# Kernel tuning notes

Measured on AMD Instinct MI355X. Metric: run time of the kernel, lower is better.

## Reference

```python
import jax, jax.numpy as jnp
import numpy as np

BS, CS, PS, D_INPUT, H, D = 4, 1024, 1024, 1024, 16, 64
T = CS + PS  # total key length
SCALE = 1.0 / D ** 0.5


def _rel_shift(x):
    # x: (bs, cs, T, H) -- faithful reshape-based relative shift
    zero_pad = jnp.zeros((*x.shape[:2], 1, x.shape[-1]), dtype=x.dtype)
    return jnp.concatenate([zero_pad, x], axis=2).reshape(
        (x.shape[2] + 1, *x.shape[:2], x.shape[-1]))[1:].reshape(x.shape)


def setup_inputs() -> dict:
    key = jax.random.key(0)
    ks = jax.random.split(key, 9)
    s = 1.0 / np.sqrt(D_INPUT)
    input_ = jax.random.normal(ks[0], (BS, CS, D_INPUT), jnp.float32)
    pos_embs = jax.random.normal(ks[1], (T, D_INPUT), jnp.float32)
    memory = jax.random.normal(ks[2], (BS, PS, D_INPUT), jnp.float32)
    u = jax.random.normal(ks[3], (H, D), jnp.float32) * 0.02
    v = jax.random.normal(ks[4], (H, D), jnp.float32) * 0.02
    W_kv = jax.random.normal(ks[5], (D_INPUT, 2 * H * D), jnp.float32) * s
    W_q = jax.random.normal(ks[6], (D_INPUT, H * D), jnp.float32) * s
    W_p = jax.random.normal(ks[7], (D_INPUT, H * D), jnp.float32) * s
    W_out = jax.random.normal(ks[8], (H * D, D_INPUT), jnp.float32) * (1.0 / np.sqrt(H * D))
    # causal mask: query i may attend to key j iff j <= i + prev_seq. True = keep.
    mask = (jnp.arange(T)[None, :] <= jnp.arange(CS)[:, None] + PS)[..., None]  # (cs, T, 1)
    return {"input_": input_, "pos_embs": pos_embs, "memory": memory,
            "u": u, "v": v, "W_kv": W_kv, "W_q": W_q, "W_p": W_p,
            "W_out": W_out, "mask": mask}


def reference(input_, pos_embs, memory, u, v, W_kv, W_q, W_p, W_out, mask):
    bs, cs, _ = input_.shape
    ps = memory.shape[1]
    t = cs + ps
    input_with_memory = jnp.concatenate([memory, input_], axis=1)  # (bs, T, d_input)
    kv = input_with_memory @ W_kv                                  # (bs, T, 2*H*D)
    k_tfmd, v_tfmd = jnp.split(kv, 2, axis=-1)
    q_tfmd = input_ @ W_q                                          # (bs, cs, H*D)
    q = q_tfmd.reshape(bs, cs, H, D)
    k = k_tfmd.reshape(bs, t, H, D)
    content_attn = jnp.einsum('bihd,bjhd->bijh', q + u, k)
    p_tfmd = (pos_embs @ W_p).reshape(t, H, D)
    position_attn = jnp.einsum('bihd,jhd->bijh', q + v, p_tfmd)
    position_attn = _rel_shift(position_attn)
    attn = content_attn + position_attn                            # (bs, cs, T, H)
    attn = jnp.where(jnp.broadcast_to(mask[None], attn.shape), attn, -1e30)
    attn = jax.nn.softmax(attn * SCALE, axis=2)
    vals = v_tfmd.reshape(bs, t, H, D)
    awv = jnp.einsum('bijh,bjhd->bihd', attn, vals).reshape(bs, cs, H * D)
    return awv @ W_out                                             # (bs, cs, d_input)
```

## Files before the change

kernel.cpp:

```cpp
#include <hip/hip_runtime.h>

typedef unsigned short u16;
typedef __attribute__((ext_vector_type(8))) short short8;
typedef __attribute__((ext_vector_type(4))) float float4v;

#define SCL2 (0.125f * 1.44269504088896340736f)
#define NEG_BIG -1.0e8f

#define ROR16(x, N) __int_as_float(__builtin_amdgcn_mov_dpp( \
    __float_as_int(x), 0x120 + (N), 0xF, 0xF, true))

static __device__ __forceinline__ u16 f2bf(float f) {
  union { float f; unsigned u; } x; x.f = f;
  unsigned r = x.u + 0x7fffu + ((x.u >> 16) & 1u);
  return (u16)(r >> 16);
}
static __device__ __forceinline__ float bf2f(u16 b) {
  union { unsigned u; float f; } x; x.u = ((unsigned)b) << 16;
  return x.f;
}
static __device__ __forceinline__ u16 f2h(float f) {
  union { u16 u; _Float16 h; } x; x.h = (_Float16)f; return x.u;
}

__global__ void detect_dtype(const unsigned* __restrict__ in0, int* __restrict__ flag) {
  if (threadIdx.x == 0 && blockIdx.x == 0) {
    int cnt = 0;
    for (int i = 0; i < 256; ++i) {
      unsigned e = (in0[i] >> 7) & 0xFFu;
      if (e >= 100u && e <= 140u) cnt++;
    }
    flag[0] = (cnt < 128) ? 1 : 0;
  }
}

__global__ __launch_bounds__(256) void prep_all(
    const void* __restrict__ A0, const void* __restrict__ A1, const void* __restrict__ A2,
    u16* __restrict__ O0, u16* __restrict__ O1, u16* __restrict__ O2,
    const void* __restrict__ W0, const void* __restrict__ W1,
    const void* __restrict__ W2, const void* __restrict__ W3,
    u16* __restrict__ T0, u16* __restrict__ T1,
    u16* __restrict__ T2, u16* __restrict__ T3,
    const int* __restrict__ dflag) {
  __shared__ __align__(16) u16 t[32][33];
  const int bid = blockIdx.x, tid = threadIdx.x;
  const int f32 = dflag[0];

  if (bid < 10240) {
    int z = (bid < 4096) ? 0 : (bid < 8192) ? 1 : 2;
    int lb = bid - ((z == 0) ? 0 : (z == 1) ? 4096 : 8192);
    const void* in = (z == 0) ? A0 : (z == 1) ? A1 : A2;
    u16* out = (z == 0) ? O0 : (z == 1) ? O1 : O2;
    int i = (lb * 256 + tid) * 4;
    if (f32) {
      float4 v = *(const float4*)((const float*)in + i);
      u16 o[4] = {f2bf(v.x), f2bf(v.y), f2bf(v.z), f2bf(v.w)};
      *(uint2*)(out + i) = *(uint2*)o;
    } else {
      *(uint2*)(out + i) = *(const uint2*)((const u16*)in + i);
    }
    return;
  }
  int z, lb;
  if (bid < 12288)      { z = 0; lb = bid - 10240; }
  else if (bid < 13312) { z = 1; lb = bid - 12288; }
  else if (bid < 14336) { z = 2; lb = bid - 13312; }
  else                  { z = 3; lb = bid - 14336; }
  const void* in = (z == 0) ? W0 : (z == 1) ? W1 : (z == 2) ? W2 : W3;
  u16* out = (z == 0) ? T0 : (z == 1) ? T1 : (z == 2) ? T2 : T3;
  const int C = (z == 0) ? 2048 : 1024;
  const int nbx = C / 32;
  const int bx = lb % nbx, by = lb / nbx;
  const int tx = tid & 31, ty = tid >> 5;
  int c = bx * 32 + tx;
  int rbase = by * 32;
#pragma unroll
  for (int k = 0; k < 4; ++k) {
    int r = rbase + ty + k * 8;
    size_t idx = (size_t)r * C + c;
    t[ty + k * 8][tx] = f32 ? f2bf(((const float*)in)[idx]) : ((const u16*)in)[idx];
  }
  __syncthreads();
  int r2 = rbase + tx;
#pragma unroll
  for (int k = 0; k < 4; ++k) {
    int c2 = bx * 32 + ty + k * 8;
    out[(size_t)c2 * 1024 + r2] = t[tx][ty + k * 8];
  }
}

static __device__ __forceinline__ const u16* gemm_arow(
    const u16* A, const u16* gmem, const u16* ginp,
    int lda, long aOff, long aZ, int z, int rg) {
  if (A) return A + (size_t)rg * lda + aOff + (long)z * aZ;
  int bb = rg >> 11, t = rg & 2047;
  return (t < 1024) ? (gmem + ((size_t)(bb * 1024 + t)) * 1024)
                    : (ginp + ((size_t)(bb * 1024 + t - 1024)) * 1024);
}

__global__ __launch_bounds__(256) void gemm_proj(
    const u16* __restrict__ memB, const u16* __restrict__ inpB,
    const u16* __restrict__ poseB,
    const u16* __restrict__ WkvT, const u16* __restrict__ WqT,
    const u16* __restrict__ WpT,
    u16* __restrict__ Kb, u16* __restrict__ VT,
    u16* __restrict__ QU, u16* __restrict__ QV, u16* __restrict__ Pb,
    const void* __restrict__ ub, const void* __restrict__ vb,
    const int* __restrict__ dflag, int K)
{
  __shared__ __align__(16) u16 As[2][128][40];
  __shared__ __align__(16) u16 Bs[2][128][40];
  const int f32g = dflag[0];
  const int tid = threadIdx.x;
  const int w = tid >> 6, lane = tid & 63, quad = lane >> 4, l15 = lane & 15;
  const int wr = w >> 1, wc = w & 1;
  const int srow = tid >> 2, sc8 = (tid & 3) * 8;

  const int bid = blockIdx.x;
  int prob, bx, by;
  if (bid < 1024)      { prob = 0; bx = bid & 15; by = bid >> 4; }
  else if (bid < 1280) { int t = bid - 1024; prob = 1; bx = t & 7; by = t >> 3; }
  else                 { int t = bid - 1280; prob = 2; bx = t & 7; by = t >> 3; }
  const int m0 = by * 128, n0 = bx * 128;
  const u16* BT = (prob == 0) ? WkvT : (prob == 1) ? WqT : WpT;

  const u16 *apr0, *apr1;
  if (prob == 0) {
    apr0 = gemm_arow(nullptr, memB, inpB, 0, 0, 0, 0, m0 + srow) + sc8;
    apr1 = gemm_arow(nullptr, memB, inpB, 0, 0, 0, 0, m0 + 64 + srow) + sc8;
  } else {
    const u16* Ab = (prob == 1) ? inpB : poseB;
    apr0 = Ab + (size_t)(m0 + srow) * 1024 + sc8;
    apr1 = Ab + (size_t)(m0 + 64 + srow) * 1024 + sc8;
  }
  const u16* bpr0 = BT + (size_t)(n0 + srow) * 1024 + sc8;
  const u16* bpr1 = BT + (size_t)(n0 + 64 + srow) * 1024 + sc8;

  float4v acc[4][4];
#pragma unroll
  for (int i = 0; i < 4; ++i)
#pragma unroll
    for (int j = 0; j < 4; ++j) acc[i][j] = (float4v){0.f, 0.f, 0.f, 0.f};

  uint4 aR0 = *(const uint4*)(apr0);
  uint4 aR1 = *(const uint4*)(apr1);
  uint4 bR0 = *(const uint4*)(bpr0);
  uint4 bR1 = *(const uint4*)(bpr1);

  int p = 0;
  for (int kt = 0; kt < K; kt += 32, p ^= 1) {
    *(uint4*)&As[p][srow][sc8] = aR0;
    *(uint4*)&As[p][64 + srow][sc8] = aR1;
    *(uint4*)&Bs[p][srow][sc8] = bR0;
    *(uint4*)&Bs[p][64 + srow][sc8] = bR1;
    __syncthreads();
    if (kt + 32 < K) {
      aR0 = *(const uint4*)(apr0 + kt + 32);
      aR1 = *(const uint4*)(apr1 + kt + 32);
      bR0 = *(const uint4*)(bpr0 + kt + 32);
      bR1 = *(const uint4*)(bpr1 + kt + 32);
    }
    short8 af[4], bf[4];
#pragma unroll
    for (int mi = 0; mi < 4; ++mi)
      af[mi] = *(const short8*)&As[p][wr * 64 + mi * 16 + l15][quad * 8];
#pragma unroll
    for (int ni = 0; ni < 4; ++ni)
      bf[ni] = *(const short8*)&Bs[p][wc * 64 + ni * 16 + l15][quad * 8];
#pragma unroll
    for (int mi = 0; mi < 4; ++mi)
#pragma unroll
      for (int ni = 0; ni < 4; ++ni)
        acc[mi][ni] = __builtin_amdgcn_mfma_f32_16x16x32_bf16(af[mi], bf[ni], acc[mi][ni], 0, 0, 0);
  }

#pragma unroll
  for (int mi = 0; mi < 4; ++mi) {
#pragma unroll
    for (int ni = 0; ni < 4; ++ni) {
      int rg0 = m0 + wr * 64 + mi * 16 + quad * 4;
      int cg = n0 + wc * 64 + ni * 16 + l15;
      if (prob == 0) {
        if (cg >= 1024) {
          int d_full = cg - 1024;
          int hh = d_full >> 6, dd = d_full & 63;
          int niv = dd >> 4, lv = dd & 15;
          int bb = rg0 >> 11, t0 = rg0 & 2047;
          int jt = t0 >> 7, tp = t0 & 127;
          int f = ((tp >> 5) << 2) + niv;
          int lanev = ((tp >> 3) & 3) * 16 + lv;
          int iv = tp & 7;
          size_t Aidx = ((((size_t)(bb * 16 + hh) * 16 + jt) * 16 + f) * 64 + lanev) * 8 + iv;
          u16 h4[4] = {f2h(acc[mi][ni][0]), f2h(acc[mi][ni][1]),
                       f2h(acc[mi][ni][2]), f2h(acc[mi][ni][3])};
          *(uint2*)&VT[Aidx] = *(uint2*)h4;
        } else {
#pragma unroll
          for (int r = 0; r < 4; ++r)
            Kb[(size_t)(rg0 + r) * 1024 + cg] = f2bf(acc[mi][ni][r]);
        }
      } else if (prob == 1) {
        float uu = f32g ? ((const float*)ub)[cg] : bf2f(((const u16*)ub)[cg]);
        float vv = f32g ? ((const float*)vb)[cg] : bf2f(((const u16*)vb)[cg]);
#pragma unroll
        for (int r = 0; r < 4; ++r) {
          size_t ci = (size_t)(rg0 + r) * 1024 + cg;
          QU[ci] = f2bf(acc[mi][ni][r] + uu);
          QV[ci] = f2bf(acc[mi][ni][r] + vv);
        }
      } else {
#pragma unroll
        for (int r = 0; r < 4; ++r)
          Pb[(size_t)(rg0 + r) * 1024 + cg] = f2bf(acc[mi][ni][r]);
      }
    }
  }
}

__global__ __launch_bounds__(256) void gemm_out(
    const u16* __restrict__ A, const u16* __restrict__ BT,
    void* __restrict__ Cp, const int* __restrict__ dflag)
{
  __shared__ __align__(16) u16 As[2][64][40];
  __shared__ __align__(16) u16 Bs[2][128][40];
  const int f32g = dflag[0];
  const int tid = threadIdx.x;
  const int w = tid >> 6, lane = tid & 63, quad = lane >> 4, l15 = lane & 15;
  const int wr = w >> 1, wc = w & 1;
  const int m0 = blockIdx.y * 64, n0 = blockIdx.x * 128;
  const int srow = tid >> 2, sc8 = (tid & 3) * 8;

  const u16* apr0 = A + (size_t)(m0 + srow) * 1024 + sc8;
  const u16* bpr0 = BT + (size_t)(n0 + srow) * 1024 + sc8;
  const u16* bpr1 = BT + (size_t)(n0 + 64 + srow) * 1024 + sc8;

  float4v acc[2][4];
#pragma unroll
  for (int i = 0; i < 2; ++i)
#pragma unroll
    for (int j = 0; j < 4; ++j) acc[i][j] = (float4v){0.f, 0.f, 0.f, 0.f};

  uint4 aR0 = *(const uint4*)(apr0);
  uint4 bR0 = *(const uint4*)(bpr0);
  uint4 bR1 = *(const uint4*)(bpr1);

  int p = 0;
  for (int kt = 0; kt < 1024; kt += 32, p ^= 1) {
    *(uint4*)&As[p][srow][sc8] = aR0;
    *(uint4*)&Bs[p][srow][sc8] = bR0;
    *(uint4*)&Bs[p][64 + srow][sc8] = bR1;
    __syncthreads();
    if (kt + 32 < 1024) {
      aR0 = *(const uint4*)(apr0 + kt + 32);
      bR0 = *(const uint4*)(bpr0 + kt + 32);
      bR1 = *(const uint4*)(bpr1 + kt + 32);
    }
    short8 af[2], bf[4];
#pragma unroll
    for (int mi = 0; mi < 2; ++mi)
      af[mi] = *(const short8*)&As[p][wr * 32 + mi * 16 + l15][quad * 8];
#pragma unroll
    for (int ni = 0; ni < 4; ++ni)
      bf[ni] = *(const short8*)&Bs[p][wc * 64 + ni * 16 + l15][quad * 8];
#pragma unroll
    for (int mi = 0; mi < 2; ++mi)
#pragma unroll
      for (int ni = 0; ni < 4; ++ni)
        acc[mi][ni] = __builtin_amdgcn_mfma_f32_16x16x32_bf16(af[mi], bf[ni], acc[mi][ni], 0, 0, 0);
  }

#pragma unroll
  for (int mi = 0; mi < 2; ++mi) {
#pragma unroll
    for (int ni = 0; ni < 4; ++ni) {
      int rg0 = m0 + wr * 32 + mi * 16 + quad * 4;
      int cg = n0 + wc * 64 + ni * 16 + l15;
#pragma unroll
      for (int r = 0; r < 4; ++r) {
        size_t ci = (size_t)(rg0 + r) * 1024 + cg;
        float va = acc[mi][ni][r];
        if (f32g) ((float*)Cp)[ci] = va;
        else      ((u16*)Cp)[ci] = f2bf(va);
      }
    }
  }
}

#define BLD(itc) ({ \
  int dd_ = ddmN + (itc) * 32 + trow; \
  int q2_ = (dd_ >= 2049) + (dd_ >= 4098); \
  int jp_ = dd_ - 2049 * q2_; \
  uint4 pv_ = *(const uint4*)(PbH + (size_t)((jp_ > 0) ? jp_ - 1 : 0) * 1024); \
  uint4 z4_ = {0u, 0u, 0u, 0u}; \
  (jp_ == 0) ? z4_ : pv_; })

#define KSB(row, cb) ((char*)Ks + (size_t)(row) * 128 + ((cb) ^ (((row) & 7) << 4)))

#define BANDFRAG(fc, dst) { \
      int dds = ddminW + (fc) * 16; \
      int qlo = (dds >= 2049) + (dds >= 4098); \
      int qhi = (dds + 15 >= 2049) + (dds + 15 >= 4098); \
      if (qlo != q2c) { \
        const u16* ar = &qvs[16 * w + l15 + qlo][0]; \
        a0 = *(const short8*)(ar + quad * 8); \
        a1 = *(const short8*)(ar + 32 + quad * 8); \
        q2c = qlo; \
      } \
      const u16* br = &band[(toff + (fc) * 16 + l15) * 72]; \
      short8 b0 = *(const short8*)(br + quad * 8); \
      short8 b1 = *(const short8*)(br + 32 + quad * 8); \
      float4v c = (float4v){0.f, 0.f, 0.f, 0.f}; \
      c = __builtin_amdgcn_mfma_f32_16x16x32_bf16(a0, b0, c, 0, 0, 0); \
      c = __builtin_amdgcn_mfma_f32_16x16x32_bf16(a1, b1, c, 0, 0, 0); \
      if (qhi != qlo) { \
        const u16* ar2 = &qvs[16 * w + l15 + qhi][0]; \
        short8 e0 = *(const short8*)(ar2 + quad * 8); \
        short8 e1 = *(const short8*)(ar2 + 32 + quad * 8); \
        float4v c2 = (float4v){0.f, 0.f, 0.f, 0.f}; \
        c2 = __builtin_amdgcn_mfma_f32_16x16x32_bf16(e0, b0, c2, 0, 0, 0); \
        c2 = __builtin_amdgcn_mfma_f32_16x16x32_bf16(e1, b1, c2, 0, 0, 0); \
        int colX = ((qlo == 0) ? 2049 : 4098) - dds; \
        bool useHi = (l15 >= colX); \
        for (int rr = 0; rr < 4; ++rr) c[rr] = useHi ? c2[rr] : c[rr]; \
      } \
      dst = c; }

__global__ __launch_bounds__(256, 2) void attn_fused(
    const u16* __restrict__ QU, const u16* __restrict__ QV,
    const u16* __restrict__ Kb, const u16* __restrict__ VT,
    const u16* __restrict__ Pb, u16* __restrict__ AWV)
{
  __shared__ __align__(16) u16 band[192 * 72];
  __shared__ __align__(16) u16 Ks[128 * 64];
  __shared__ __align__(16) u16 qvs[66][72];
  __shared__ __align__(16) u16 Ps[4 * 16 * 72];
  const int b = blockIdx.z, h = blockIdx.y;
  const int i0 = (15 - blockIdx.x) * 64;
  const int tid = threadIdx.x, w = tid >> 6, lane = tid & 63;
  const int quad = lane >> 4, l15 = lane & 15;
  const int iw = i0 + w * 16;
  const int m0 = b * 1024 + i0;
  const int MQ = 5120 - 1024 * b;

  const size_t qb = ((size_t)(b * 1024 + iw + l15)) * 1024 + h * 64 + quad * 8;
  short8 qf0 = *(const short8*)(QU + qb);
  short8 qf1 = *(const short8*)(QU + qb + 32);

#pragma unroll
  for (int it = 0; it < 3; ++it) {
    int slot = it * 256 + tid;
    if (slot < 528) {
      int row = slot >> 3, d8q = (slot & 7) * 8;
      int gr = m0 + row; if (gr > 4095) gr = 4095;
      *(uint4*)&qvs[row][d8q] = *(const uint4*)(QV + (size_t)gr * 1024 + h * 64 + d8q);
    }
  }

  float4v o[4];
#pragma unroll
  for (int ni = 0; ni < 4; ++ni) o[ni] = (float4v){0.f, 0.f, 0.f, 0.f};
  float mrun[4] = {NEG_BIG, NEG_BIG, NEG_BIG, NEG_BIG};
  float lrun[4] = {0.f, 0.f, 0.f, 0.f};

  const int toff = 48 - 16 * w;
  const int nT = (i0 + 1088 + 127) / 128;

  const int trow = tid >> 3, d8 = (tid & 7) * 8;
  const u16* PbH = Pb + h * 64 + d8;
  const u16* KbH = Kb + ((size_t)(b * 2048 + trow)) * 1024 + h * 64 + d8;
  const u16* Vg = VT + (size_t)(b * 16 + h) * 131072 + (size_t)lane * 8;
  const int ddm0 = 4096 - m0 - 63 + trow;

  int ddmN = ddm0 - trow;
  uint4 bRa = BLD(0), bRb = BLD(1), bRc = BLD(2), bRd = BLD(3), bRe = BLD(4), bRf = BLD(5);
  uint4 kRa = *(const uint4*)(KbH);
  uint4 kRb = *(const uint4*)(KbH + 32 * 1024);
  uint4 kRc = *(const uint4*)(KbH + 64 * 1024);
  uint4 kRd = *(const uint4*)(KbH + 96 * 1024);

  for (int jt = 0; jt < nT; ++jt) {
    const int j0 = jt * 128;
    const int ddminB = j0 + 4096 - (m0 + 63);
    const u16* VgT = Vg + (size_t)jt * 8192;

    *(uint4*)&band[(0 * 32 + trow) * 72 + d8] = bRa;
    *(uint4*)&band[(1 * 32 + trow) * 72 + d8] = bRb;
    *(uint4*)&band[(2 * 32 + trow) * 72 + d8] = bRc;
    *(uint4*)&band[(3 * 32 + trow) * 72 + d8] = bRd;
    *(uint4*)&band[(4 * 32 + trow) * 72 + d8] = bRe;
    *(uint4*)&band[(5 * 32 + trow) * 72 + d8] = bRf;
    *(uint4*)KSB(0 * 32 + trow, (tid & 7) * 16) = kRa;
    *(uint4*)KSB(1 * 32 + trow, (tid & 7) * 16) = kRb;
    *(uint4*)KSB(2 * 32 + trow, (tid & 7) * 16) = kRc;
    *(uint4*)KSB(3 * 32 + trow, (tid & 7) * 16) = kRd;
    __syncthreads();

    if (jt + 1 < nT) {
      const int j0n = j0 + 128;
      ddmN = j0n + 4096 - m0 - 63;
      bRa = BLD(0); bRb = BLD(1); bRc = BLD(2);
      bRd = BLD(3); bRe = BLD(4); bRf = BLD(5);
      const u16* kp = KbH + (size_t)j0n * 1024;
      kRa = *(const uint4*)(kp);
      kRb = *(const uint4*)(kp + 32 * 1024);
      kRc = *(const uint4*)(kp + 64 * 1024);
      kRd = *(const uint4*)(kp + 96 * 1024);
    }

    float4v sc[8];
    __builtin_amdgcn_s_setprio(1);
#pragma unroll
    for (int nj = 0; nj < 8; ++nj) {
      const int kr = nj * 16 + l15;
      short8 bk0 = *(const short8*)KSB(kr, quad * 16);
      short8 bk1 = *(const short8*)KSB(kr, 64 + quad * 16);
      float4v s = (float4v){0.f, 0.f, 0.f, 0.f};
      s = __builtin_amdgcn_mfma_f32_16x16x32_bf16(qf0, bk0, s, 0, 0, 0);
      s = __builtin_amdgcn_mfma_f32_16x16x32_bf16(qf1, bk1, s, 0, 0, 0);
      sc[nj] = s;
    }

    const int ddminW = ddminB + toff;
    const int tmaxW = MQ - ddminW;
    float4v bc[5];
    int q2c = -1;
    short8 a0, a1;
    BANDFRAG(0, bc[0])
    BANDFRAG(1, bc[1])
    BANDFRAG(2, bc[2])
    BANDFRAG(3, bc[3])
    BANDFRAG(4, bc[4])
    __builtin_amdgcn_s_setprio(0);
#pragma unroll
    for (int r = 0; r < 4; ++r) {
      const int tb = 15 - quad * 4 - r;
      const int adr = 4 * (((l15 + tb) & 15) + 16 * quad);
      const bool srcHi = (l15 < tb);
#pragma unroll
      for (int nj = 0; nj < 4; ++nj) {
        float mg = srcHi ? bc[nj + 1][r] : bc[nj][r];
        int p = __builtin_amdgcn_ds_bpermute(adr, __float_as_int(mg));
        float pos = __int_as_float(p);
        float v2 = (sc[nj][r] + pos) * SCL2;
        int tw = nj * 16 + l15 + tb;
        sc[nj][r] = (tw <= tmaxW) ? v2 : NEG_BIG;
      }
    }
    bc[0] = bc[4];
    __builtin_amdgcn_s_setprio(1);
    BANDFRAG(5, bc[1])
    BANDFRAG(6, bc[2])
    BANDFRAG(7, bc[3])
    BANDFRAG(8, bc[4])
    __builtin_amdgcn_s_setprio(0);
#pragma unroll
    for (int r = 0; r < 4; ++r) {
      const int tb = 15 - quad * 4 - r;
      const int adr = 4 * (((l15 + tb) & 15) + 16 * quad);
      const bool srcHi = (l15 < tb);
#pragma unroll
      for (int nj = 4; nj < 8; ++nj) {
        float mg = srcHi ? bc[nj - 3][r] : bc[nj - 4][r];
        int p = __builtin_amdgcn_ds_bpermute(adr, __float_as_int(mg));
        float pos = __int_as_float(p);
        float v2 = (sc[nj][r] + pos) * SCL2;
        int tw = nj * 16 + l15 + tb;
        sc[nj][r] = (tw <= tmaxW) ? v2 : NEG_BIG;
      }
    }

    short8 va0 = *(const short8*)(VgT);
    short8 va1 = *(const short8*)(VgT + 512);
    short8 va2 = *(const short8*)(VgT + 1024);
    short8 va3 = *(const short8*)(VgT + 1536);

#pragma unroll
    for (int r = 0; r < 4; ++r) {
      float mx = sc[0][r];
#pragma unroll
      for (int nj = 1; nj < 8; ++nj) mx = fmaxf(mx, sc[nj][r]);
      mx = fmaxf(mx, ROR16(mx, 8));
      mx = fmaxf(mx, ROR16(mx, 4));
      mx = fmaxf(mx, ROR16(mx, 2));
      mx = fmaxf(mx, ROR16(mx, 1));
      float mnew = fmaxf(mrun[r], mx);
      float al = exp2f(mrun[r] - mnew);
      float rs = 0.f;
#pragma unroll
      for (int nj = 0; nj < 8; ++nj) {
        float pv = exp2f(sc[nj][r] - mnew);
        sc[nj][r] = pv;
        rs += pv;
      }
      rs += ROR16(rs, 8);
      rs += ROR16(rs, 4);
      rs += ROR16(rs, 2);
      rs += ROR16(rs, 1);
      lrun[r] = lrun[r] * al + rs;
      mrun[r] = mnew;
#pragma unroll
      for (int ni = 0; ni < 4; ++ni) o[ni][r] *= al;
    }

    short8 vb0 = *(const short8*)(VgT + 2048);
    short8 vb1 = *(const short8*)(VgT + 2560);
    short8 vb2 = *(const short8*)(VgT + 3072);
    short8 vb3 = *(const short8*)(VgT + 3584);

    u16* Psw = Ps + w * 1152;
#pragma unroll
    for (int nj = 0; nj < 4; ++nj)
#pragma unroll
      for (int r = 0; r < 4; ++r)
        Psw[(quad * 4 + r) * 72 + nj * 16 + l15] = f2h(sc[nj][r]);
    {
      short8 ap = *(const short8*)&Psw[l15 * 72 + quad * 8];
      __builtin_amdgcn_s_setprio(1);
      o[0] = __builtin_amdgcn_mfma_f32_16x16x32_f16(ap, va0, o[0], 0, 0, 0);
      o[1] = __builtin_amdgcn_mfma_f32_16x16x32_f16(ap, va1, o[1], 0, 0, 0);
      o[2] = __builtin_amdgcn_mfma_f32_16x16x32_f16(ap, va2, o[2], 0, 0, 0);
      o[3] = __builtin_amdgcn_mfma_f32_16x16x32_f16(ap, va3, o[3], 0, 0, 0);
      __builtin_amdgcn_s_setprio(0);
    }
    va0 = *(const short8*)(VgT + 4096);
    va1 = *(const short8*)(VgT + 4608);
    va2 = *(const short8*)(VgT + 5120);
    va3 = *(const short8*)(VgT + 5632);
    {
      short8 ap = *(const short8*)&Psw[l15 * 72 + 32 + quad * 8];
      __builtin_amdgcn_s_setprio(1);
      o[0] = __builtin_amdgcn_mfma_f32_16x16x32_f16(ap, vb0, o[0], 0, 0, 0);
      o[1] = __builtin_amdgcn_mfma_f32_16x16x32_f16(ap, vb1, o[1], 0, 0, 0);
      o[2] = __builtin_amdgcn_mfma_f32_16x16x32_f16(ap, vb2, o[2], 0, 0, 0);
      o[3] = __builtin_amdgcn_mfma_f32_16x16x32_f16(ap, vb3, o[3], 0, 0, 0);
      __builtin_amdgcn_s_setprio(0);
    }
    vb0 = *(const short8*)(VgT + 6144);
    vb1 = *(const short8*)(VgT + 6656);
    vb2 = *(const short8*)(VgT + 7168);
    vb3 = *(const short8*)(VgT + 7680);
#pragma unroll
    for (int nj = 0; nj < 4; ++nj)
#pragma unroll
      for (int r = 0; r < 4; ++r)
        Psw[(quad * 4 + r) * 72 + nj * 16 + l15] = f2h(sc[4 + nj][r]);
    {
      short8 ap = *(const short8*)&Psw[l15 * 72 + quad * 8];
      __builtin_amdgcn_s_setprio(1);
      o[0] = __builtin_amdgcn_mfma_f32_16x16x32_f16(ap, va0, o[0], 0, 0, 0);
      o[1] = __builtin_amdgcn_mfma_f32_16x16x32_f16(ap, va1, o[1], 0, 0, 0);
      o[2] = __builtin_amdgcn_mfma_f32_16x16x32_f16(ap, va2, o[2], 0, 0, 0);
      o[3] = __builtin_amdgcn_mfma_f32_16x16x32_f16(ap, va3, o[3], 0, 0, 0);
      __builtin_amdgcn_s_setprio(0);
    }
    {
      short8 ap = *(const short8*)&Psw[l15 * 72 + 32 + quad * 8];
      __builtin_amdgcn_s_setprio(1);
      o[0] = __builtin_amdgcn_mfma_f32_16x16x32_f16(ap, vb0, o[0], 0, 0, 0);
      o[1] = __builtin_amdgcn_mfma_f32_16x16x32_f16(ap, vb1, o[1], 0, 0, 0);
      o[2] = __builtin_amdgcn_mfma_f32_16x16x32_f16(ap, vb2, o[2], 0, 0, 0);
      o[3] = __builtin_amdgcn_mfma_f32_16x16x32_f16(ap, vb3, o[3], 0, 0, 0);
      __builtin_amdgcn_s_setprio(0);
    }
    __syncthreads();
  }

#pragma unroll
  for (int r = 0; r < 4; ++r) {
    float inv = 1.0f / lrun[r];
#pragma unroll
    for (int ni = 0; ni < 4; ++ni) {
      AWV[((size_t)(b * 1024 + iw + quad * 4 + r)) * 1024 + h * 64 + ni * 16 + l15] =
          f2bf(o[ni][r] * inv);
    }
  }
}

extern "C" void kernel_launch(void* const* d_in, const int* in_sizes, int n_in,
                              void* d_out, int out_size, void* d_ws, size_t ws_size,
                              hipStream_t stream) {
  const void* input_ = d_in[0];
  const void* pose   = d_in[1];
  const void* memry  = d_in[2];
  const void* ubias  = d_in[3];
  const void* vbias  = d_in[4];
  const void* Wkv    = d_in[5];
  const void* Wq     = d_in[6];
  const void* Wp     = d_in[7];
  const void* Wout   = d_in[8];

  char* base = (char*)d_ws;
  size_t off = 0;
  auto carve = [&](size_t bytes) {
    void* r = base + off;
    off += (bytes + 255) & ~(size_t)255;
    return r;
  };
  int* dflag = (int*)carve(256);
  u16* Kb    = (u16*)carve((size_t)4 * 2048 * 1024 * 2);
  u16* VT    = (u16*)carve((size_t)1024 * 4 * 2048 * 2);
  u16* QU    = (u16*)carve((size_t)4 * 1024 * 1024 * 2);
  u16* QV    = (u16*)carve((size_t)4 * 1024 * 1024 * 2);
  u16* Pb    = (u16*)carve((size_t)2048 * 1024 * 2);
  u16* AWVb  = (u16*)carve((size_t)4 * 1024 * 1024 * 2);
  u16* WkvT  = (u16*)carve((size_t)2048 * 1024 * 2);
  u16* WqT   = (u16*)carve((size_t)1024 * 1024 * 2);
  u16* WpT   = (u16*)carve((size_t)1024 * 1024 * 2);
  u16* WoutT = (u16*)carve((size_t)1024 * 1024 * 2);
  u16* inpB  = (u16*)carve((size_t)4 * 1024 * 1024 * 2);
  u16* memB  = (u16*)carve((size_t)4 * 1024 * 1024 * 2);
  u16* poseB = (u16*)carve((size_t)2048 * 1024 * 2);

  detect_dtype<<<1, 64, 0, stream>>>((const unsigned*)input_, dflag);
  prep_all<<<dim3(15360, 1, 1), 256, 0, stream>>>(
      input_, memry, pose, inpB, memB, poseB,
      Wkv, Wq, Wp, Wout, WkvT, WqT, WpT, WoutT, dflag);

  gemm_proj<<<dim3(1408, 1, 1), 256, 0, stream>>>(
      memB, inpB, poseB, WkvT, WqT, WpT,
      Kb, VT, QU, QV, Pb, ubias, vbias, dflag, 1024);

  attn_fused<<<dim3(16, 16, 4), 256, 0, stream>>>(QU, QV, Kb, VT, Pb, AWVb);

  gemm_out<<<dim3(8, 64, 1), 256, 0, stream>>>(AWVb, WoutT, d_out, dflag);
}
```

Measured before the change: 378.8 us.

## Store K in MFMA-fragment layout and load B operands directly into registers

The projection GEMM epilogue now writes K in a per-(batch, head, tile) fragment-ordered layout matching the MFMA B-operand lane mapping, as was already done for V. The attention kernel drops the K LDS tile and its swizzled stores and reads, loading 16 short8 fragments per lane straight from global memory and prefetching the next tile after the QK MFMAs. This removes LDS traffic and bank pressure for K, at the cost of 64 extra VGPRs per lane holding fragments, which may reduce occupancy under launch_bounds(256,2). Each wave also reloads the full K tile independently, so global and L2 traffic for K grows, and the epilogue's 2-byte scattered stores may be less coalesced.

```diff
diff --git a/kernel.cpp b/kernel.cpp
--- a/kernel.cpp
+++ b/kernel.cpp
@@ -181,12 +181,12 @@
       int rg0 = m0 + wr * 64 + mi * 16 + quad * 4;
       int cg = n0 + wc * 64 + ni * 16 + l15;
       if (prob == 0) {
+        int bb = rg0 >> 11, t0 = rg0 & 2047;
+        int jt = t0 >> 7, tp = t0 & 127;
         if (cg >= 1024) {
           int d_full = cg - 1024;
           int hh = d_full >> 6, dd = d_full & 63;
           int niv = dd >> 4, lv = dd & 15;
-          int bb = rg0 >> 11, t0 = rg0 & 2047;
-          int jt = t0 >> 7, tp = t0 & 127;
           int f = ((tp >> 5) << 2) + niv;
           int lanev = ((tp >> 3) & 3) * 16 + lv;
           int iv = tp & 7;
@@ -195,9 +195,15 @@
                        f2h(acc[mi][ni][2]), f2h(acc[mi][ni][3])};
           *(uint2*)&VT[Aidx] = *(uint2*)h4;
         } else {
-#pragma unroll
-          for (int r = 0; r < 4; ++r)
-            Kb[(size_t)(rg0 + r) * 1024 + cg] = f2bf(acc[mi][ni][r]);
+          int hh = cg >> 6, dd = cg & 63;
+          int kk = dd >> 5, qv_ = (dd >> 3) & 3, iv = dd & 7;
+          size_t base = (((size_t)(bb * 16 + hh) * 16 + jt) * 16 + kk * 8);
+#pragma unroll
+          for (int r = 0; r < 4; ++r) {
+            int tpr = tp + r;
+            int njr = tpr >> 4, l15r = tpr & 15;
+            Kb[((base + njr) * 64 + qv_ * 16 + l15r) * 8 + iv] = f2bf(acc[mi][ni][r]);
+          }
         }
       } else if (prob == 1) {
         float uu = f32g ? ((const float*)ub)[cg] : bf2f(((const u16*)ub)[cg]);
@@ -293,8 +299,6 @@
   uint4 pv_ = *(const uint4*)(PbH + (size_t)((jp_ > 0) ? jp_ - 1 : 0) * 1024); \
   uint4 z4_ = {0u, 0u, 0u, 0u}; \
   (jp_ == 0) ? z4_ : pv_; })
-
-#define KSB(row, cb) ((char*)Ks + (size_t)(row) * 128 + ((cb) ^ (((row) & 7) << 4)))
 
 #define BANDFRAG(fc, dst) { \
       int dds = ddminW + (fc) * 16; \
@@ -331,7 +335,6 @@
     const u16* __restrict__ Pb, u16* __restrict__ AWV)
 {
   __shared__ __align__(16) u16 band[192 * 72];
-  __shared__ __align__(16) u16 Ks[128 * 64];
   __shared__ __align__(16) u16 qvs[66][72];
   __shared__ __align__(16) u16 Ps[4 * 16 * 72];
   const int b = blockIdx.z, h = blockIdx.y;
@@ -367,16 +370,15 @@
 
   const int trow = tid >> 3, d8 = (tid & 7) * 8;
   const u16* PbH = Pb + h * 64 + d8;
-  const u16* KbH = Kb + ((size_t)(b * 2048 + trow)) * 1024 + h * 64 + d8;
+  const u16* Kf = Kb + (size_t)(b * 16 + h) * 131072 + (size_t)lane * 8;
   const u16* Vg = VT + (size_t)(b * 16 + h) * 131072 + (size_t)lane * 8;
   const int ddm0 = 4096 - m0 - 63 + trow;
 
   int ddmN = ddm0 - trow;
   uint4 bRa = BLD(0), bRb = BLD(1), bRc = BLD(2), bRd = BLD(3), bRe = BLD(4), bRf = BLD(5);
-  uint4 kRa = *(const uint4*)(KbH);
-  uint4 kRb = *(const uint4*)(KbH + 32 * 1024);
-  uint4 kRc = *(const uint4*)(KbH + 64 * 1024);
-  uint4 kRd = *(const uint4*)(KbH + 96 * 1024);
+  short8 kf[16];
+#pragma unroll
+  for (int f = 0; f < 16; ++f) kf[f] = *(const short8*)(Kf + f * 512);
 
   for (int jt = 0; jt < nT; ++jt) {
     const int j0 = jt * 128;
@@ -389,35 +391,29 @@
     *(uint4*)&band[(3 * 32 + trow) * 72 + d8] = bRd;
     *(uint4*)&band[(4 * 32 + trow) * 72 + d8] = bRe;
     *(uint4*)&band[(5 * 32 + trow) * 72 + d8] = bRf;
-    *(uint4*)KSB(0 * 32 + trow, (tid & 7) * 16) = kRa;
-    *(uint4*)KSB(1 * 32 + trow, (tid & 7) * 16) = kRb;
-    *(uint4*)KSB(2 * 32 + trow, (tid & 7) * 16) = kRc;
-    *(uint4*)KSB(3 * 32 + trow, (tid & 7) * 16) = kRd;
     __syncthreads();
 
     if (jt + 1 < nT) {
-      const int j0n = j0 + 128;
-      ddmN = j0n + 4096 - m0 - 63;
+      ddmN = j0 + 128 + 4096 - m0 - 63;
       bRa = BLD(0); bRb = BLD(1); bRc = BLD(2);
       bRd = BLD(3); bRe = BLD(4); bRf = BLD(5);
-      const u16* kp = KbH + (size_t)j0n * 1024;
-      kRa = *(const uint4*)(kp);
-      kRb = *(const uint4*)(kp + 32 * 1024);
-      kRc = *(const uint4*)(kp + 64 * 1024);
-      kRd = *(const uint4*)(kp + 96 * 1024);
     }
 
     float4v sc[8];
     __builtin_amdgcn_s_setprio(1);
 #pragma unroll
     for (int nj = 0; nj < 8; ++nj) {
-      const int kr = nj * 16 + l15;
-      short8 bk0 = *(const short8*)KSB(kr, quad * 16);
-      short8 bk1 = *(const short8*)KSB(kr, 64 + quad * 16);
       float4v s = (float4v){0.f, 0.f, 0.f, 0.f};
-      s = __builtin_amdgcn_mfma_f32_16x16x32_bf16(qf0, bk0, s, 0, 0, 0);
-      s = __builtin_amdgcn_mfma_f32_16x16x32_bf16(qf1, bk1, s, 0, 0, 0);
+      s = __builtin_amdgcn_mfma_f32_16x16x32_bf16(qf0, kf[nj], s, 0, 0, 0);
+      s = __builtin_amdgcn_mfma_f32_16x16x32_bf16(qf1, kf[8 + nj], s, 0, 0, 0);
       sc[nj] = s;
+    }
+    __builtin_amdgcn_s_setprio(0);
+
+    if (jt + 1 < nT) {
+      const u16* KfT = Kf + (size_t)(jt + 1) * 8192;
+#pragma unroll
+      for (int f = 0; f < 16; ++f) kf[f] = *(const short8*)(KfT + f * 512);
     }
 
     const int ddminW = ddminB + toff;
@@ -425,6 +421,7 @@
     float4v bc[5];
     int q2c = -1;
     short8 a0, a1;
+    __builtin_amdgcn_s_setprio(1);
     BANDFRAG(0, bc[0])
     BANDFRAG(1, bc[1])
     BANDFRAG(2, bc[2])
```

Result: slower. 390.6 us (+3.1%).
